# Kernel tuning notes

Measured on AMD Instinct MI355X. Metric: run time of the kernel, lower is better.

Reference implementation:

```python
import jax, jax.numpy as jnp
import numpy as np

BATCH, L = 2, 1024
D_MODEL, D_INNER, D_STATE, DT_RANK, K = 2048, 4096, 16, 128, 4


def setup_inputs() -> dict:
    key = jax.random.key(0)
    ks = jax.random.split(key, 9)
    g = lambda i, shape, s: jax.random.normal(ks[i], shape, jnp.float32) * s
    A_log = jnp.log(jnp.broadcast_to(jnp.arange(1, D_STATE + 1, dtype=jnp.float32),
                                     (D_INNER, D_STATE)))
    return {
        "hidden_states": g(0, (BATCH, L, D_MODEL), 1.0),
        "W_in": g(1, (2 * D_INNER, D_MODEL), 0.02),
        "conv_w": g(2, (D_INNER, K), 0.2),
        "conv_b": g(3, (D_INNER,), 0.02),
        "W_x": g(4, (DT_RANK + 2 * D_STATE, D_INNER), 0.02),
        "W_dt": g(5, (D_INNER, DT_RANK), 0.02),
        "b_dt": g(6, (D_INNER,), 0.02),
        "A_log": A_log,
        "D": jnp.ones((D_INNER,), jnp.float32),
        "W_out": g(7, (D_MODEL, D_INNER), 0.02),
        "b_out": g(8, (D_MODEL,), 0.02),
    }


def reference(hidden_states, W_in, conv_w, conv_b, W_x, W_dt, b_dt, A_log, D, W_out, b_out):
    b, l, _ = hidden_states.shape
    # in_proj -> (b, 2*d_inner, l), split into x and gate z
    xz = jnp.einsum('bld,ed->bel', hidden_states, W_in)
    x, z = jnp.split(xz, 2, axis=1)                      # each (b, d_inner, l)
    # conv_state = F.pad(x, (d_conv - l, 0)): keeps the last d_conv timesteps
    conv_state = x[:, :, -K:]
    # causal depthwise conv1d (left pad K-1) + SiLU
    xc = jax.lax.conv_general_dilated(
        x, conv_w[:, None, :], window_strides=(1,), padding=[(K - 1, 0)],
        feature_group_count=D_INNER, dimension_numbers=('NCH', 'OIH', 'NCH'))
    xc = jax.nn.silu(xc + conv_b[None, :, None])         # (b, d_inner, l)
    # x_proj -> dt / B / C
    x_dbl = jnp.einsum('bdl,ed->ble', xc, W_x)           # (b, l, dt_rank+2n)
    dt, Bm, Cm = jnp.split(x_dbl, [DT_RANK, DT_RANK + D_STATE], axis=-1)
    dt = jnp.einsum('blr,dr->bdl', dt, W_dt)             # (b, d_inner, l), no bias here
    delta = jax.nn.softplus(dt + b_dt[None, :, None])    # dt_proj bias folded into softplus
    A = -jnp.exp(A_log)                                  # (d_inner, d_state)

    def step(state, inp):                                # state: (b, d_inner, d_state)
        d_t, b_t, c_t, u_t = inp                         # (b,d), (b,n), (b,n), (b,d)
        dA = jnp.exp(d_t[..., None] * A)                 # (b, d, n)
        state = dA * state + (d_t * u_t)[..., None] * b_t[:, None, :]
        y_t = jnp.einsum('bdn,bn->bd', state, c_t)
        return state, y_t

    xs = (delta.transpose(2, 0, 1),                      # (l, b, d)
          Bm.transpose(1, 0, 2),                         # (l, b, n)
          Cm.transpose(1, 0, 2),
          xc.transpose(2, 0, 1))
    init = jnp.zeros((b, D_INNER, D_STATE), delta.dtype)
    last_state, ys = jax.lax.scan(step, init, xs)
    y = ys.transpose(1, 2, 0) + D[None, :, None] * xc    # (b, d_inner, l) skip term
    y = y * jax.nn.silu(z)                               # gating
    out = jnp.einsum('bdl,ed->ble', y, W_out) + b_out    # (b, l, d_model)
    return out, conv_state, last_state
```

## Files before the change

kernel.cpp:

```cpp
#include <hip/hip_runtime.h>
#include <stdint.h>
#include <stddef.h>

typedef __bf16 bf16;
typedef __attribute__((ext_vector_type(8))) __bf16 bf16x8;
typedef __attribute__((ext_vector_type(4))) float floatx4;

#define GAS __attribute__((address_space(1)))
#define LAS __attribute__((address_space(3)))

__device__ __forceinline__ void async16(const void* g, void* l) {
  __builtin_amdgcn_global_load_lds((const GAS void*)g, (LAS void*)l, 16, 0, 0);
}

__device__ __forceinline__ bf16x8 cvt8(const float* p) {
  floatx4 a = *(const floatx4*)p;
  floatx4 b = *(const floatx4*)(p + 4);
  bf16x8 r;
  r[0] = (bf16)a[0]; r[1] = (bf16)a[1]; r[2] = (bf16)a[2]; r[3] = (bf16)a[3];
  r[4] = (bf16)b[0]; r[5] = (bf16)b[1]; r[6] = (bf16)b[2]; r[7] = (bf16)b[3];
  return r;
}

template <int EPI, int AF, int BF, int TM>
__global__ __launch_bounds__(256, 2) void gemm_bt(
    const void* __restrict__ Aptr, const void* __restrict__ Bptr,
    void* __restrict__ Cout, const float* __restrict__ bias,
    int M, int N, int K, int lda, int ldb) {
  __shared__ bf16 As[TM * 32];
  __shared__ bf16 Bs[128 * 32];
  const int tid = threadIdx.x;

  const int rowBase = blockIdx.x * TM;
  const int colBase = blockIdx.y * 128;
  const int kLen = K / gridDim.z;
  const int k0 = blockIdx.z * kLen;
  const int kIters = kLen / 32;

  const int sRow = tid >> 2;
  const int sCol = (tid & 3) << 3;
  const int wave = tid >> 6;
  const int lane = tid & 63;
  constexpr int MI = 4;
  constexpr int NJ = (TM == 128) ? 4 : 2;
  const int wm = (TM == 128) ? ((wave >> 1) << 6) : 0;
  const int wn = (TM == 128) ? ((wave & 1) << 6) : (wave << 5);
  const int lr = lane & 15;
  const int kg = lane >> 4;

  floatx4 acc[MI][NJ] = {};

  for (int kt = 0; kt < kIters; ++kt) {
    const int kk = k0 + kt * 32;
    __syncthreads();
    if constexpr (AF) {
      const float* pa =
          (const float*)Aptr + (size_t)(rowBase + sRow) * lda + kk + sCol;
      *(bf16x8*)&As[tid * 8] = cvt8(pa);
      if constexpr (TM == 128)
        *(bf16x8*)&As[2048 + tid * 8] = cvt8(pa + (size_t)64 * lda);
    } else {
      const bf16* pa =
          (const bf16*)Aptr + (size_t)(rowBase + sRow) * lda + kk + sCol;
      async16(pa, &As[tid * 8]);
      if constexpr (TM == 128)
        async16(pa + (size_t)64 * lda, &As[2048 + tid * 8]);
    }
    if constexpr (BF) {
      const float* pb =
          (const float*)Bptr + (size_t)(colBase + sRow) * ldb + kk + sCol;
      *(bf16x8*)&Bs[tid * 8] = cvt8(pb);
      *(bf16x8*)&Bs[2048 + tid * 8] = cvt8(pb + (size_t)64 * ldb);
    } else {
      const bf16* pb =
          (const bf16*)Bptr + (size_t)(colBase + sRow) * ldb + kk + sCol;
      async16(pb, &Bs[tid * 8]);
      async16(pb + (size_t)64 * ldb, &Bs[2048 + tid * 8]);
    }
    __syncthreads();

    bf16x8 af[MI], bg[NJ];
#pragma unroll
    for (int i = 0; i < MI; ++i)
      af[i] = *(const bf16x8*)&As[(wm + i * 16 + lr) * 32 + kg * 8];
#pragma unroll
    for (int j = 0; j < NJ; ++j)
      bg[j] = *(const bf16x8*)&Bs[(wn + j * 16 + lr) * 32 + kg * 8];
#pragma unroll
    for (int i = 0; i < MI; ++i)
#pragma unroll
      for (int j = 0; j < NJ; ++j)
        acc[i][j] = __builtin_amdgcn_mfma_f32_16x16x32_bf16(af[i], bg[j],
                                                            acc[i][j], 0, 0, 0);
  }

#pragma unroll
  for (int i = 0; i < MI; ++i) {
#pragma unroll
    for (int j = 0; j < NJ; ++j) {
      const int col = colBase + wn + j * 16 + lr;
      float bv = 0.f;
      if constexpr (EPI == 2 || EPI == 3) bv = bias[col];
#pragma unroll
      for (int r = 0; r < 4; ++r) {
        const int row = rowBase + wm + i * 16 + kg * 4 + r;
        const size_t idx = (size_t)row * N + col;
        float v = acc[i][j][r];
        if constexpr (EPI == 0) {
          ((bf16*)Cout)[idx] = (bf16)v;
        } else if constexpr (EPI == 1) {
          atomicAdd((float*)Cout + idx, v);
        } else if constexpr (EPI == 2) {
          v += bv;
          const float t = __expf(v);
          const float sp = (v > 20.f) ? v : __logf(1.f + t);
          ((bf16*)Cout)[idx] = (bf16)sp;
        } else {
          ((float*)Cout)[idx] = v + bv;
        }
      }
    }
  }
}

#define PC0 524288UL
#define PC1 2621440UL
#define PC2 2686976UL
#define PC3 3735552UL
#define PC4 3866624UL
#define PC5 3932160UL
__global__ __launch_bounds__(256) void prep_all(
    const float* __restrict__ h, const float* __restrict__ wi,
    const float* __restrict__ wd, const float* __restrict__ wo,
    const float* __restrict__ wx, bf16* __restrict__ hb,
    bf16* __restrict__ wib, bf16* __restrict__ wdb, bf16* __restrict__ wob,
    bf16* __restrict__ wxp, float* __restrict__ xdbl) {
  const size_t c = (size_t)blockIdx.x * 256 + threadIdx.x;
  if (c < PC0) {
    const size_t e = c * 8;
    *(bf16x8*)&hb[e] = cvt8(&h[e]);
  } else if (c < PC1) {
    const size_t e = (c - PC0) * 8;
    *(bf16x8*)&wib[e] = cvt8(&wi[e]);
  } else if (c < PC2) {
    const size_t e = (c - PC1) * 8;
    *(bf16x8*)&wdb[e] = cvt8(&wd[e]);
  } else if (c < PC3) {
    const size_t e = (c - PC2) * 8;
    *(bf16x8*)&wob[e] = cvt8(&wo[e]);
  } else if (c < PC4) {
    const size_t e = (c - PC3) * 8;
    if ((e >> 12) < 160) {
      *(bf16x8*)&wxp[e] = cvt8(&wx[e]);
    } else {
      bf16x8 z = {};
      *(bf16x8*)&wxp[e] = z;
    }
  } else {
    const size_t e = (c - PC4) * 8;
    floatx4 z = {};
    *(floatx4*)&xdbl[e] = z;
    *(floatx4*)&xdbl[e + 4] = z;
  }
}

__global__ void wxpad_prep(const float* __restrict__ Wx,
                           bf16* __restrict__ WXPAD) {
  const int idx = blockIdx.x * 256 + threadIdx.x;
  const int row = idx >> 12;
  WXPAD[idx] = (row < 160) ? (bf16)Wx[idx] : (bf16)0.f;
}

__global__ void conv_kernel(const bf16* __restrict__ XZ,
                            const float* __restrict__ conv_w,
                            const float* __restrict__ conv_b,
                            bf16* __restrict__ XC,
                            float* __restrict__ outConv) {
  const int idx = blockIdx.x * 256 + threadIdx.x;
  const int d = idx & 4095;
  const int row = idx >> 12;
  const int l = row & 1023;
  float acc = conv_b[d];
#pragma unroll
  for (int k = 0; k < 4; ++k) {
    if (l - 3 + k >= 0)
      acc += conv_w[d * 4 + k] * (float)XZ[(size_t)(row - 3 + k) * 8192 + d];
  }
  const float s = acc / (1.f + __expf(-acc));
  XC[(size_t)row * 4096 + d] = (bf16)s;
  if (idx < 32768) {
    const int k = idx & 3;
    const int dd = (idx >> 2) & 4095;
    const int b = idx >> 14;
    outConv[idx] = (float)XZ[(size_t)(b * 1024 + 1020 + k) * 8192 + dd];
  }
}

#define NCH 32
#define CLEN 32
#define LOG2E 1.44269504088896f

__global__ __launch_bounds__(256) void scan_phase1(
    const bf16* __restrict__ DELTA, const bf16* __restrict__ XC,
    const float* __restrict__ XDBL, const float* __restrict__ A_log,
    bf16* __restrict__ P, bf16* __restrict__ Lc) {
  const int bd = blockIdx.x * 256 + threadIdx.x;
  const int c = blockIdx.y;
  const int b = bd >> 12;
  const int d = bd & 4095;
  float A2[16], st[16], p[16];
#pragma unroll
  for (int n = 0; n < 16; ++n) {
    A2[n] = -__expf(A_log[d * 16 + n]) * LOG2E;
    st[n] = 0.f;
    p[n] = 1.f;
  }
  size_t row = (size_t)b * 1024 + (size_t)c * CLEN;
  for (int t = 0; t < CLEN; ++t, ++row) {
    const float dlt = (float)DELTA[row * 4096 + d];
    const float u = (float)XC[row * 4096 + d];
    const float* __restrict__ Bp = XDBL + row * 256 + 128;
    const float du = dlt * u;
#pragma unroll
    for (int n = 0; n < 16; ++n) {
      const float dA = exp2f(dlt * A2[n]);
      st[n] = dA * st[n] + du * Bp[n];
      p[n] *= dA;
    }
  }
  const size_t o = ((size_t)c * 8192 + bd) * 16;
  bf16x8 pk[2], lk[2];
#pragma unroll
  for (int n = 0; n < 16; ++n) {
    pk[n >> 3][n & 7] = (bf16)p[n];
    lk[n >> 3][n & 7] = (bf16)st[n];
  }
  *(bf16x8*)&P[o] = pk[0];
  *(bf16x8*)&P[o + 8] = pk[1];
  *(bf16x8*)&Lc[o] = lk[0];
  *(bf16x8*)&Lc[o + 8] = lk[1];
}

__global__ __launch_bounds__(256) void scan_phase2(
    const bf16* __restrict__ P, const bf16* __restrict__ Lc,
    float* __restrict__ In, float* __restrict__ lastOut) {
  const int bd = blockIdx.x * 256 + threadIdx.x;
  float st[16] = {};
  for (int c = 0; c < NCH; ++c) {
    const size_t o = ((size_t)c * 8192 + bd) * 16;
    const bf16x8 p0 = *(const bf16x8*)&P[o];
    const bf16x8 p1 = *(const bf16x8*)&P[o + 8];
    const bf16x8 l0 = *(const bf16x8*)&Lc[o];
    const bf16x8 l1 = *(const bf16x8*)&Lc[o + 8];
    floatx4 w[4];
#pragma unroll
    for (int n = 0; n < 16; ++n) w[n >> 2][n & 3] = st[n];
#pragma unroll
    for (int q = 0; q < 4; ++q) *(floatx4*)&In[o + q * 4] = w[q];
#pragma unroll
    for (int n = 0; n < 8; ++n) {
      st[n] = (float)p0[n] * st[n] + (float)l0[n];
      st[8 + n] = (float)p1[n] * st[8 + n] + (float)l1[n];
    }
  }
  const int b = bd >> 12;
  const int d = bd & 4095;
#pragma unroll
  for (int n = 0; n < 16; ++n)
    lastOut[(size_t)b * 65536 + d * 16 + n] = st[n];
}

__global__ __launch_bounds__(256) void scan_phase3(
    const bf16* __restrict__ DELTA, const bf16* __restrict__ XC,
    const bf16* __restrict__ XZ, const float* __restrict__ XDBL,
    const float* __restrict__ A_log, const float* __restrict__ Dp,
    const float* __restrict__ In, bf16* __restrict__ Y) {
  const int bd = blockIdx.x * 256 + threadIdx.x;
  const int c = blockIdx.y;
  const int b = bd >> 12;
  const int d = bd & 4095;
  float A2[16], st[16];
  const size_t o = ((size_t)c * 8192 + bd) * 16;
#pragma unroll
  for (int q = 0; q < 4; ++q) {
    const floatx4 v = *(const floatx4*)&In[o + q * 4];
#pragma unroll
    for (int j = 0; j < 4; ++j) st[q * 4 + j] = v[j];
  }
#pragma unroll
  for (int n = 0; n < 16; ++n)
    A2[n] = -__expf(A_log[d * 16 + n]) * LOG2E;
  const float Dd = Dp[d];
  size_t row = (size_t)b * 1024 + (size_t)c * CLEN;
  for (int t = 0; t < CLEN; ++t, ++row) {
    const float dlt = (float)DELTA[row * 4096 + d];
    const float u = (float)XC[row * 4096 + d];
    const float z = (float)XZ[row * 8192 + 4096 + d];
    const float* __restrict__ Bp = XDBL + row * 256 + 128;
    const float du = dlt * u;
    float y = 0.f;
#pragma unroll
    for (int n = 0; n < 16; ++n) {
      const float dA = exp2f(dlt * A2[n]);
      st[n] = dA * st[n] + du * Bp[n];
      y += st[n] * Bp[16 + n];
    }
    const float sig = 1.f / (1.f + __expf(-z));
    Y[row * 4096 + d] = (bf16)((y + Dd * u) * (z * sig));
  }
}

#define OFF_XZ 0UL
#define OFF_XC 33554432UL
#define OFF_DELTA 50331648UL
#define OFF_Y 83886080UL
#define OFF_XDBL 100663296UL
#define OFF_WXPAD 103284736UL
#define OFF_P 105381888UL
#define OFF_L 113770496UL
#define OFF_HBF 122159104UL
#define OFF_WINBF 130547712UL
#define OFF_WDTBF 164102144UL
#define OFF_WOUTBF 165150720UL
#define WS_NEED_CAST 181927936UL

extern "C" void kernel_launch(void* const* d_in, const int* in_sizes, int n_in,
                              void* d_out, int out_size, void* d_ws,
                              size_t ws_size, hipStream_t stream) {
  const float* hidden = (const float*)d_in[0];
  const float* W_in = (const float*)d_in[1];
  const float* conv_w = (const float*)d_in[2];
  const float* conv_b = (const float*)d_in[3];
  const float* W_x = (const float*)d_in[4];
  const float* W_dt = (const float*)d_in[5];
  const float* b_dt = (const float*)d_in[6];
  const float* A_log = (const float*)d_in[7];
  const float* Dvec = (const float*)d_in[8];
  const float* W_out = (const float*)d_in[9];
  const float* b_out = (const float*)d_in[10];

  char* ws = (char*)d_ws;
  bf16* XZ = (bf16*)(ws + OFF_XZ);
  bf16* XC = (bf16*)(ws + OFF_XC);
  bf16* DELTA = (bf16*)(ws + OFF_DELTA);
  bf16* Y = (bf16*)(ws + OFF_Y);
  float* XDBL = (float*)(ws + OFF_XDBL);
  bf16* WXPAD = (bf16*)(ws + OFF_WXPAD);
  bf16* P = (bf16*)(ws + OFF_P);
  bf16* Lc = (bf16*)(ws + OFF_L);

  float* out = (float*)d_out;
  float* out_conv = out + 4194304;
  float* out_last = out + 4227072;
  float* In = out;

  const bool castOK = ws_size >= WS_NEED_CAST;
  if (castOK) {
    bf16* HBF = (bf16*)(ws + OFF_HBF);
    bf16* WINBF = (bf16*)(ws + OFF_WINBF);
    bf16* WDTBF = (bf16*)(ws + OFF_WDTBF);
    bf16* WOUTBF = (bf16*)(ws + OFF_WOUTBF);
    prep_all<<<15360, 256, 0, stream>>>(hidden, W_in, W_dt, W_out, W_x, HBF,
                                        WINBF, WDTBF, WOUTBF, WXPAD, XDBL);
    gemm_bt<0, 0, 0, 128><<<dim3(16, 64, 1), 256, 0, stream>>>(
        HBF, WINBF, XZ, nullptr, 2048, 8192, 2048, 2048, 2048);
    conv_kernel<<<32768, 256, 0, stream>>>(XZ, conv_w, conv_b, XC, out_conv);
    gemm_bt<1, 0, 0, 128><<<dim3(16, 2, 16), 256, 0, stream>>>(
        XC, WXPAD, XDBL, nullptr, 2048, 256, 4096, 4096, 4096);
    gemm_bt<2, 1, 0, 64><<<dim3(32, 32, 1), 256, 0, stream>>>(
        XDBL, WDTBF, DELTA, b_dt, 2048, 4096, 128, 256, 128);
    scan_phase1<<<dim3(32, NCH), 256, 0, stream>>>(DELTA, XC, XDBL, A_log, P,
                                                   Lc);
    scan_phase2<<<32, 256, 0, stream>>>(P, Lc, In, out_last);
    scan_phase3<<<dim3(32, NCH), 256, 0, stream>>>(DELTA, XC, XZ, XDBL, A_log,
                                                   Dvec, In, Y);
    gemm_bt<3, 0, 0, 64><<<dim3(32, 16, 1), 256, 0, stream>>>(
        Y, WOUTBF, out, b_out, 2048, 2048, 4096, 4096, 4096);
  } else {
    wxpad_prep<<<4096, 256, 0, stream>>>(W_x, WXPAD);
    hipMemsetAsync(XDBL, 0, 2048UL * 256 * 4, stream);
    gemm_bt<0, 1, 1, 128><<<dim3(16, 64, 1), 256, 0, stream>>>(
        hidden, W_in, XZ, nullptr, 2048, 8192, 2048, 2048, 2048);
    conv_kernel<<<32768, 256, 0, stream>>>(XZ, conv_w, conv_b, XC, out_conv);
    gemm_bt<1, 0, 0, 128><<<dim3(16, 2, 16), 256, 0, stream>>>(
        XC, WXPAD, XDBL, nullptr, 2048, 256, 4096, 4096, 4096);
    gemm_bt<2, 1, 1, 64><<<dim3(32, 32, 1), 256, 0, stream>>>(
        XDBL, W_dt, DELTA, b_dt, 2048, 4096, 128, 256, 128);
    scan_phase1<<<dim3(32, NCH), 256, 0, stream>>>(DELTA, XC, XDBL, A_log, P,
                                                   Lc);
    scan_phase2<<<32, 256, 0, stream>>>(P, Lc, In, out_last);
    scan_phase3<<<dim3(32, NCH), 256, 0, stream>>>(DELTA, XC, XZ, XDBL, A_log,
                                                   Dvec, In, Y);
    gemm_bt<3, 0, 1, 64><<<dim3(32, 16, 1), 256, 0, stream>>>(
        Y, W_out, out, b_out, 2048, 2048, 4096, 4096, 4096);
  }
}
```

Measured before the change: 536.5 us.

## Replace atomic split-K x_proj with partial buffers plus reduction; retune tiles and occupancy

The x_proj GEMM no longer accumulates split-K results with float atomics into a zeroed buffer. Each of 8 K-slices now writes its own partial tile, and a new reduce kernel sums them, which also removes the XDBL zeroing from prep and the memset. The launch bounds hint for the GEMM rises from 2 to 4 blocks per CU, which may force register spills. The out-projection moves from 64-row to 128-row tiles. The partial buffer is placed past DELTA in the workspace, which assumes that region is free and large enough.

```diff
diff --git a/kernel.cpp b/kernel.cpp
--- a/kernel.cpp
+++ b/kernel.cpp
@@ -23,7 +23,7 @@
 }
 
 template <int EPI, int AF, int BF, int TM>
-__global__ __launch_bounds__(256, 2) void gemm_bt(
+__global__ __launch_bounds__(256, 4) void gemm_bt(
     const void* __restrict__ Aptr, const void* __restrict__ Bptr,
     void* __restrict__ Cout, const float* __restrict__ bias,
     int M, int N, int K, int lda, int ldb) {
@@ -115,12 +115,26 @@
           const float t = __expf(v);
           const float sp = (v > 20.f) ? v : __logf(1.f + t);
           ((bf16*)Cout)[idx] = (bf16)sp;
+        } else if constexpr (EPI == 3) {
+          ((float*)Cout)[idx] = v + bv;
         } else {
-          ((float*)Cout)[idx] = v + bv;
+          ((float*)Cout)[(size_t)blockIdx.z * 524288 + idx] = v;
         }
       }
     }
   }
+}
+
+__global__ __launch_bounds__(256) void reduce_xdbl(
+    const float* __restrict__ part, float* __restrict__ xdbl) {
+  const size_t i4 = ((size_t)blockIdx.x * 256 + threadIdx.x) * 4;
+  floatx4 s = {};
+#pragma unroll
+  for (int z = 0; z < 8; ++z) {
+    const floatx4 v = *(const floatx4*)&part[(size_t)z * 524288 + i4];
+    s[0] += v[0]; s[1] += v[1]; s[2] += v[2]; s[3] += v[3];
+  }
+  *(floatx4*)&xdbl[i4] = s;
 }
 
 #define PC0 524288UL
@@ -128,13 +142,12 @@
 #define PC2 2686976UL
 #define PC3 3735552UL
 #define PC4 3866624UL
-#define PC5 3932160UL
 __global__ __launch_bounds__(256) void prep_all(
     const float* __restrict__ h, const float* __restrict__ wi,
     const float* __restrict__ wd, const float* __restrict__ wo,
     const float* __restrict__ wx, bf16* __restrict__ hb,
     bf16* __restrict__ wib, bf16* __restrict__ wdb, bf16* __restrict__ wob,
-    bf16* __restrict__ wxp, float* __restrict__ xdbl) {
+    bf16* __restrict__ wxp) {
   const size_t c = (size_t)blockIdx.x * 256 + threadIdx.x;
   if (c < PC0) {
     const size_t e = c * 8;
@@ -156,11 +169,6 @@
       bf16x8 z = {};
       *(bf16x8*)&wxp[e] = z;
     }
-  } else {
-    const size_t e = (c - PC4) * 8;
-    floatx4 z = {};
-    *(floatx4*)&xdbl[e] = z;
-    *(floatx4*)&xdbl[e + 4] = z;
   }
 }
 
@@ -343,6 +351,7 @@
   bf16* XZ = (bf16*)(ws + OFF_XZ);
   bf16* XC = (bf16*)(ws + OFF_XC);
   bf16* DELTA = (bf16*)(ws + OFF_DELTA);
+  float* PART = (float*)(ws + OFF_DELTA + 16777216UL);
   bf16* Y = (bf16*)(ws + OFF_Y);
   float* XDBL = (float*)(ws + OFF_XDBL);
   bf16* WXPAD = (bf16*)(ws + OFF_WXPAD);
@@ -360,13 +369,14 @@
     bf16* WINBF = (bf16*)(ws + OFF_WINBF);
     bf16* WDTBF = (bf16*)(ws + OFF_WDTBF);
     bf16* WOUTBF = (bf16*)(ws + OFF_WOUTBF);
-    prep_all<<<15360, 256, 0, stream>>>(hidden, W_in, W_dt, W_out, W_x, HBF,
-                                        WINBF, WDTBF, WOUTBF, WXPAD, XDBL);
+    prep_all<<<15104, 256, 0, stream>>>(hidden, W_in, W_dt, W_out, W_x, HBF,
+                                        WINBF, WDTBF, WOUTBF, WXPAD);
     gemm_bt<0, 0, 0, 128><<<dim3(16, 64, 1), 256, 0, stream>>>(
         HBF, WINBF, XZ, nullptr, 2048, 8192, 2048, 2048, 2048);
     conv_kernel<<<32768, 256, 0, stream>>>(XZ, conv_w, conv_b, XC, out_conv);
-    gemm_bt<1, 0, 0, 128><<<dim3(16, 2, 16), 256, 0, stream>>>(
-        XC, WXPAD, XDBL, nullptr, 2048, 256, 4096, 4096, 4096);
+    gemm_bt<4, 0, 0, 64><<<dim3(32, 2, 8), 256, 0, stream>>>(
+        XC, WXPAD, PART, nullptr, 2048, 256, 4096, 4096, 4096);
+    reduce_xdbl<<<512, 256, 0, stream>>>(PART, XDBL);
     gemm_bt<2, 1, 0, 64><<<dim3(32, 32, 1), 256, 0, stream>>>(
         XDBL, WDTBF, DELTA, b_dt, 2048, 4096, 128, 256, 128);
     scan_phase1<<<dim3(32, NCH), 256, 0, stream>>>(DELTA, XC, XDBL, A_log, P,
@@ -374,16 +384,16 @@
     scan_phase2<<<32, 256, 0, stream>>>(P, Lc, In, out_last);
     scan_phase3<<<dim3(32, NCH), 256, 0, stream>>>(DELTA, XC, XZ, XDBL, A_log,
                                                    Dvec, In, Y);
-    gemm_bt<3, 0, 0, 64><<<dim3(32, 16, 1), 256, 0, stream>>>(
+    gemm_bt<3, 0, 0, 128><<<dim3(16, 16, 1), 256, 0, stream>>>(
         Y, WOUTBF, out, b_out, 2048, 2048, 4096, 4096, 4096);
   } else {
     wxpad_prep<<<4096, 256, 0, stream>>>(W_x, WXPAD);
-    hipMemsetAsync(XDBL, 0, 2048UL * 256 * 4, stream);
     gemm_bt<0, 1, 1, 128><<<dim3(16, 64, 1), 256, 0, stream>>>(
         hidden, W_in, XZ, nullptr, 2048, 8192, 2048, 2048, 2048);
     conv_kernel<<<32768, 256, 0, stream>>>(XZ, conv_w, conv_b, XC, out_conv);
-    gemm_bt<1, 0, 0, 128><<<dim3(16, 2, 16), 256, 0, stream>>>(
-        XC, WXPAD, XDBL, nullptr, 2048, 256, 4096, 4096, 4096);
+    gemm_bt<4, 0, 0, 64><<<dim3(32, 2, 8), 256, 0, stream>>>(
+        XC, WXPAD, PART, nullptr, 2048, 256, 4096, 4096, 4096);
+    reduce_xdbl<<<512, 256, 0, stream>>>(PART, XDBL);
     gemm_bt<2, 1, 1, 64><<<dim3(32, 32, 1), 256, 0, stream>>>(
         XDBL, W_dt, DELTA, b_dt, 2048, 4096, 128, 256, 128);
     scan_phase1<<<dim3(32, NCH), 256, 0, stream>>>(DELTA, XC, XDBL, A_log, P,
@@ -391,7 +401,7 @@
     scan_phase2<<<32, 256, 0, stream>>>(P, Lc, In, out_last);
     scan_phase3<<<dim3(32, NCH), 256, 0, stream>>>(DELTA, XC, XZ, XDBL, A_log,
                                                    Dvec, In, Y);
-    gemm_bt<3, 0, 1, 64><<<dim3(32, 16, 1), 256, 0, stream>>>(
+    gemm_bt<3, 0, 1, 128><<<dim3(16, 16, 1), 256, 0, stream>>>(
         Y, W_out, out, b_out, 2048, 2048, 4096, 4096, 4096);
   }
 }
```

Measured after the change: 529.9 us. About the same (-1.2%).
